# Optimization experiments

Hardware: AMD Instinct MI355X
Metric: run time of the kernel (lower is better)

## Reference

```python
import jax, jax.numpy as jnp
import numpy as np

N = 100000
E = 1600000
NEG_SLOPE = 0.2


def _gat_layer(x, src, dst, W, a_src, a_dst, b, heads, out_ch):
    n = x.shape[0]
    h = (x @ W).reshape(n, heads, out_ch)                      # [N,H,C]
    alpha_src = (h * a_src).sum(-1)                            # [N,H]
    alpha_dst = (h * a_dst).sum(-1)                            # [N,H]
    e = jax.nn.leaky_relu(alpha_src[src] + alpha_dst[dst], NEG_SLOPE)  # [E,H]
    # segment softmax over incoming edges of each destination node
    m = jax.ops.segment_max(e, dst, num_segments=n)            # [N,H]
    ex = jnp.exp(e - m[dst])
    denom = jax.ops.segment_sum(ex, dst, num_segments=n)       # [N,H]
    alpha = ex / (denom[dst] + 1e-16)                          # [E,H]
    msg = h[src] * alpha[:, :, None]                           # [E,H,C]
    out = jax.ops.segment_sum(msg, dst, num_segments=n)        # [N,H,C]
    return out.reshape(n, heads * out_ch) + b


def setup_inputs() -> dict:
    key = jax.random.key(0)
    ks = jax.random.split(key, 10)
    glorot = lambda k, shape: jax.random.normal(k, shape, jnp.float32) * np.sqrt(2.0 / (shape[0] + shape[-1]))
    x = jax.random.normal(ks[0], (N, 5), jnp.float32)
    edge_index = jax.random.randint(ks[1], (2, E), 0, N, jnp.int64)
    return {
        "x": x,
        "edge_index": edge_index,
        "W1": glorot(ks[2], (5, 64)),
        "a_src1": glorot(ks[3], (8, 8)),
        "a_dst1": glorot(ks[4], (8, 8)),
        "b1": jnp.zeros((64,), jnp.float32),
        "W2": glorot(ks[5], (64, 2)),
        "a_src2": glorot(ks[6], (1, 2)),
        "a_dst2": glorot(ks[7], (1, 2)),
        "b2": jnp.zeros((2,), jnp.float32),
    }


def reference(x, edge_index, W1, a_src1, a_dst1, b1, W2, a_src2, a_dst2, b2):
    n = x.shape[0]
    loop = jnp.arange(n, dtype=edge_index.dtype)
    src = jnp.concatenate([edge_index[0], loop])   # PyG GATConv adds self-loops
    dst = jnp.concatenate([edge_index[1], loop])
    # dropout layers are no-ops in eval mode
    h = jax.nn.elu(_gat_layer(x, src, dst, W1, a_src1, a_dst1, b1, heads=8, out_ch=8))
    out = _gat_layer(h, src, dst, W2, a_src2, a_dst2, b2, heads=1, out_ch=2)
    return jax.nn.log_softmax(out, axis=1)
```

## Files before the change

### kernel.cpp

```cpp
#include <hip/hip_runtime.h>
#include <hip/hip_fp16.h>
#include <math.h>
#include <stdint.h>

#define N_NODES 100000
#define N_EDGES 1600000
#define NEG_SLOPE 0.2f
#define LOG2E 1.44269504088896340736f

#define CB     128
#define CBBITS 7
#define NCB    ((N_NODES + CB - 1) / CB)
#define TP     2048
#define NPB    ((N_EDGES + TP - 1) / TP)
#define WINB   2560
#define NB_NODE1 ((N_NODES * 8 + 511) / 512)
#define N8     ((size_t)N_NODES * 8)
#define NTT    25

typedef int nt_int4 __attribute__((ext_vector_type(4)));

__global__ void __launch_bounds__(512) k_np(
        const int* __restrict__ src, const int* __restrict__ dst,
        int* __restrict__ ofs, unsigned* __restrict__ pairs,
        const float* __restrict__ x, const float* __restrict__ W1,
        const float* __restrict__ a_src1, const float* __restrict__ a_dst1,
        __half* __restrict__ nd, float* __restrict__ ad1) {
    __shared__ int lcnt[1024];
    __shared__ unsigned stage[TP];
    __shared__ int wred[8];
    int t = threadIdx.x;

    if (blockIdx.x >= NPB) {
        int gid  = (blockIdx.x - NPB) * 512 + t;
        int n    = gid >> 3;
        int head = gid & 7;
        if (n >= N_NODES) return;

        float xv[5];
#pragma unroll
        for (int k = 0; k < 5; ++k) xv[k] = x[n * 5 + k];

        float as = 0.f, ad = 0.f;
#pragma unroll
        for (int j = 0; j < 8; ++j) {
            int c = head * 8 + j;
            float acc = 0.f;
#pragma unroll
            for (int k = 0; k < 5; ++k) acc += xv[k] * W1[k * 64 + c];
            as += acc * a_src1[c];
            ad += acc * a_dst1[c];
        }
        nd[(size_t)n * 16 + head] = __float2half(as * LOG2E);
        ad1[n * 8 + head] = ad * LOG2E;

        if (head == 0) {
            __half2 p0 = __halves2half2(__float2half(xv[0]), __float2half(xv[1]));
            __half2 p1 = __halves2half2(__float2half(xv[2]), __float2half(xv[3]));
            __half2 p2 = __halves2half2(__float2half(xv[4]), __float2half(0.f));
            __half2 p3 = __halves2half2(__float2half(0.f), __float2half(0.f));
            __half2* xp = (__half2*)&nd[(size_t)n * 16 + 8];
            xp[0] = p0; xp[1] = p1; xp[2] = p2; xp[3] = p3;
        }
        return;
    }

    int blk = blockIdx.x;
    int base = blk * TP + t * 4;
    bool act = base < N_EDGES;
    int nE = min(TP, N_EDGES - blk * TP);

    lcnt[t] = 0; lcnt[t + 512] = 0;
    __syncthreads();

    nt_int4 s4, d4;
    int myidx[4];
    if (act) {
        s4 = __builtin_nontemporal_load((const nt_int4*)(src + base));
        d4 = __builtin_nontemporal_load((const nt_int4*)(dst + base));
#pragma unroll
        for (int j = 0; j < 4; ++j)
            myidx[j] = atomicAdd(&lcnt[d4[j] >> CBBITS], 1);
    }
    __syncthreads();

    int b0 = lcnt[t * 2], b1 = lcnt[t * 2 + 1];
    int local = b0 + b1;
    int ln = t & 63, w = t >> 6;
    int sc = local;
#pragma unroll
    for (int off = 1; off < 64; off <<= 1) {
        int u = __shfl_up(sc, off, 64);
        if (ln >= off) sc += u;
    }
    if (ln == 63) wred[w] = sc;
    __syncthreads();
    if (t < 8) {
        int v = wred[t], s = v;
#pragma unroll
        for (int off = 1; off < 8; off <<= 1) {
            int u = __shfl_up(s, off, 8);
            if ((t & 7) >= off) s += u;
        }
        wred[t] = s - v;
    }
    __syncthreads();
    int run = wred[w] + sc - local;
    lcnt[t * 2] = run; lcnt[t * 2 + 1] = run + b0;
    int* orow = ofs + (size_t)blk * (NCB + 1);
    if (t * 2     <= NCB) orow[t * 2]     = run;
    if (t * 2 + 1 <= NCB) orow[t * 2 + 1] = run + b0;
    __syncthreads();

    if (act) {
#pragma unroll
        for (int j = 0; j < 4; ++j) {
            int d = d4[j];
            stage[lcnt[d >> CBBITS] + myidx[j]] =
                ((unsigned)(d & (CB - 1)) << 17) | (unsigned)s4[j];
        }
    }
    __syncthreads();
    for (int i = t; i < nE; i += 512)
        pairs[(size_t)blk * TP + i] = stage[i];
}

__global__ void __launch_bounds__(256) k_tr(
        const int* __restrict__ ofs, int* __restrict__ ofsT) {
    __shared__ int tile[32][33];
    int bx = blockIdx.x % NTT;
    int by = blockIdx.x / NTT;
    int tx = threadIdx.x & 31, ty = threadIdx.x >> 5;
#pragma unroll
    for (int i = 0; i < 4; ++i) {
        int r = by * 32 + ty + 8 * i;
        int c = bx * 32 + tx;
        tile[ty + 8 * i][tx] = (r < NPB && c <= NCB)
                             ? ofs[(size_t)r * (NCB + 1) + c] : 0;
    }
    __syncthreads();
#pragma unroll
    for (int i = 0; i < 4; ++i) {
        int c = bx * 32 + ty + 8 * i;
        int r = by * 32 + tx;
        if (c <= NCB && r < NPB)
            ofsT[(size_t)c * NPB + r] = tile[tx][ty + 8 * i];
    }
}

__global__ void __launch_bounds__(512) k_csr(
        const int* __restrict__ ofsT, const unsigned* __restrict__ pairs,
        int* __restrict__ rbeg, int* __restrict__ rend, int* __restrict__ ssrc) {
    __shared__ unsigned stIn[WINB];
    __shared__ int stOut[WINB];
    __shared__ unsigned short sliceId[WINB];
    __shared__ int o0s[NPB];
    __shared__ int cns[1026];
    __shared__ int lcnt[CB], lofs[CB], lcur[CB];
    __shared__ int wsum[2];
    __shared__ int wred[8];
    int B = blockIdx.x, t = threadIdx.x;
    int nvalid = min(CB, N_NODES - B * CB);
    int obase = B * WINB;

    for (int s = t; s < NPB; s += 512) {
        int o0 = ofsT[(size_t)B       * NPB + s];
        int o1 = ofsT[(size_t)(B + 1) * NPB + s];
        o0s[s] = o0;
        cns[s] = o1 - o0;
    }
    for (int s = NPB + t; s < 1024; s += 512) cns[s] = 0;
    if (t < CB) {
        lcnt[t] = (t < nvalid) ? 1 : 0;
        lcur[t] = 1;
    }
    __syncthreads();

    int a0 = cns[t * 2], a1 = cns[t * 2 + 1];
    int local = a0 + a1;
    int ln = t & 63, w = t >> 6;
    int sc2 = local;
#pragma unroll
    for (int off = 1; off < 64; off <<= 1) {
        int u = __shfl_up(sc2, off, 64);
        if (ln >= off) sc2 += u;
    }
    if (ln == 63) wred[w] = sc2;
    __syncthreads();
    if (t < 8) {
        int v = wred[t], s = v;
#pragma unroll
        for (int off = 1; off < 8; off <<= 1) {
            int u = __shfl_up(s, off, 8);
            if ((t & 7) >= off) s += u;
        }
        wred[t] = s - v;
    }
    __syncthreads();
    int run = wred[w] + sc2 - local;
    cns[t * 2] = run; cns[t * 2 + 1] = run + a0;
    __syncthreads();
    int m = cns[NPB];

    for (int s = t; s < NPB; s += 512) {
        int j0 = cns[s], j1 = cns[s + 1];
        for (int j = j0; j < j1; ++j) sliceId[j] = (unsigned short)s;
    }
    __syncthreads();

    for (int i = t; i < m; i += 512) {
        int s = sliceId[i];
        unsigned r = pairs[(size_t)s * TP + o0s[s] + (i - cns[s])];
        stIn[i] = r;
        atomicAdd(&lcnt[r >> 17], 1);
    }
    __syncthreads();

    int v = (t < CB) ? lcnt[t] : 0;
    int wv = t >> 6;
    int sc = v;
#pragma unroll
    for (int off = 1; off < 64; off <<= 1) {
        int u = __shfl_up(sc, off, 64);
        if (ln >= off) sc += u;
    }
    if (ln == 63 && wv < 2) wsum[wv] = sc;
    __syncthreads();
    int wbase = (wv == 1) ? wsum[0] : 0;
    int ex = wbase + sc - v;
    if (t < CB) {
        lofs[t] = ex;
        int gi = B * CB + t;
        if (gi < N_NODES) {
            rbeg[gi] = obase + ex;
            rend[gi] = obase + ex + v;
            stOut[ex] = gi;
        }
    }
    __syncthreads();

    for (int k = t; k < m; k += 512) {
        unsigned p = stIn[k];
        int dl = p >> 17;
        int idx = atomicAdd(&lcur[dl], 1);
        stOut[lofs[dl] + idx] = (int)(p & 0x1FFFF);
    }
    __syncthreads();

    int tot = m + nvalid;
    for (int i = t; i < tot; i += 512) ssrc[obase + i] = stOut[i];
}

__global__ void __launch_bounds__(256) k_gather1(
        const int* __restrict__ rbeg, const int* __restrict__ rend,
        const int* __restrict__ ssrc, const __half* __restrict__ nd,
        const float* __restrict__ ad1, float* __restrict__ xsbuf) {
    int gtid = blockIdx.x * blockDim.x + threadIdx.x;
    int d      = gtid >> 4;
    int lane16 = threadIdx.x & 15;
    if (d >= N_NODES) return;
    int e = lane16 >> 3;
    int h = lane16 & 7;

    int beg = rbeg[d], end = rend[d];
    float adv = ad1[d * 8 + h];
    float c0 = 0.f, c1 = 0.f, c2 = 0.f, c3 = 0.f, c4 = 0.f, den = 0.f;

    for (int k = beg; k < end; k += 4) {
        int kA = k + e, kB = k + 2 + e;
        bool vA = kA < end, vB = kB < end;
        int sA = ssrc[vA ? kA : beg];
        int sB = ssrc[vB ? kB : beg];
        float eA = __half2float(nd[(size_t)sA * 16 + h]);
        float eB = __half2float(nd[(size_t)sB * 16 + h]);
        float4 xA = *(const float4*)(nd + (size_t)sA * 16 + 8);
        float4 xB = *(const float4*)(nd + (size_t)sB * 16 + 8);
        float tA = eA + adv; tA = fmaxf(tA, NEG_SLOPE * tA);
        float tB = eB + adv; tB = fmaxf(tB, NEG_SLOPE * tB);
        float wA = vA ? __builtin_amdgcn_exp2f(tA) : 0.f;
        float wB = vB ? __builtin_amdgcn_exp2f(tB) : 0.f;
        float2 A01 = __half22float2(*(__half2*)&xA.x);
        float2 A23 = __half22float2(*(__half2*)&xA.y);
        float2 A4_ = __half22float2(*(__half2*)&xA.z);
        float2 B01 = __half22float2(*(__half2*)&xB.x);
        float2 B23 = __half22float2(*(__half2*)&xB.y);
        float2 B4_ = __half22float2(*(__half2*)&xB.z);
        c0 += wA * A01.x + wB * B01.x;
        c1 += wA * A01.y + wB * B01.y;
        c2 += wA * A23.x + wB * B23.x;
        c3 += wA * A23.y + wB * B23.y;
        c4 += wA * A4_.x + wB * B4_.x;
        den += wA + wB;
    }

#define REDH(x) x += __shfl_xor(x, 8, 64);
    REDH(c0) REDH(c1) REDH(c2) REDH(c3) REDH(c4) REDH(den)
#undef REDH

    if (e == 0) {
        float inv = 1.f / den;
        size_t idx = (size_t)d * 8 + h;
        xsbuf[idx]          = c0 * inv;
        xsbuf[N8 + idx]     = c1 * inv;
        xsbuf[2 * N8 + idx] = c2 * inv;
        xsbuf[3 * N8 + idx] = c3 * inv;
        xsbuf[4 * N8 + idx] = c4 * inv;
    }
}

__global__ void __launch_bounds__(256) k_rec(
        const float* __restrict__ xsbuf, const float* __restrict__ b1,
        const float* __restrict__ W1, const float* __restrict__ W2,
        const float* __restrict__ a_src2, const float* __restrict__ a_dst2,
        float4* __restrict__ rec) {
    int gtid = blockIdx.x * blockDim.x + threadIdx.x;
    int d = gtid >> 3;
    int h = gtid & 7;
    if (d >= N_NODES) return;

    size_t idx = (size_t)d * 8 + h;
    float xs[5] = { xsbuf[idx], xsbuf[N8 + idx], xsbuf[2 * N8 + idx],
                    xsbuf[3 * N8 + idx], xsbuf[4 * N8 + idx] };

    float4 hA = ((const float4*)b1)[2 * h];
    float4 hB = ((const float4*)b1)[2 * h + 1];
#pragma unroll
    for (int c = 0; c < 5; ++c) {
        float xc = xs[c];
        float4 wA = *(const float4*)(W1 + c * 64 + 8 * h);
        float4 wB = *(const float4*)(W1 + c * 64 + 8 * h + 4);
        hA.x += xc * wA.x; hA.y += xc * wA.y; hA.z += xc * wA.z; hA.w += xc * wA.w;
        hB.x += xc * wB.x; hB.y += xc * wB.y; hB.z += xc * wB.z; hB.w += xc * wB.w;
    }
    float v0 = hA.x, v1 = hA.y, v2 = hA.z, v3 = hA.w;
    float v4 = hB.x, v5 = hB.y, v6 = hB.z, v7 = hB.w;
    v0 = (v0 > 0.f) ? v0 : (__expf(v0) - 1.f);
    v1 = (v1 > 0.f) ? v1 : (__expf(v1) - 1.f);
    v2 = (v2 > 0.f) ? v2 : (__expf(v2) - 1.f);
    v3 = (v3 > 0.f) ? v3 : (__expf(v3) - 1.f);
    v4 = (v4 > 0.f) ? v4 : (__expf(v4) - 1.f);
    v5 = (v5 > 0.f) ? v5 : (__expf(v5) - 1.f);
    v6 = (v6 > 0.f) ? v6 : (__expf(v6) - 1.f);
    v7 = (v7 > 0.f) ? v7 : (__expf(v7) - 1.f);

    const float4* w4 = (const float4*)(W2 + h * 16);
    float4 wq0 = w4[0], wq1 = w4[1], wq2 = w4[2], wq3 = w4[3];
    float h20 = v0 * wq0.x + v1 * wq0.z + v2 * wq1.x + v3 * wq1.z
              + v4 * wq2.x + v5 * wq2.z + v6 * wq3.x + v7 * wq3.z;
    float h21 = v0 * wq0.y + v1 * wq0.w + v2 * wq1.y + v3 * wq1.w
              + v4 * wq2.y + v5 * wq2.w + v6 * wq3.y + v7 * wq3.w;
    h20 += __shfl_xor(h20, 1, 64); h20 += __shfl_xor(h20, 2, 64); h20 += __shfl_xor(h20, 4, 64);
    h21 += __shfl_xor(h21, 1, 64); h21 += __shfl_xor(h21, 2, 64); h21 += __shfl_xor(h21, 4, 64);

    if (h == 0) {
        float as2v = (h20 * a_src2[0] + h21 * a_src2[1]) * LOG2E;
        float ad2v = (h20 * a_dst2[0] + h21 * a_dst2[1]) * LOG2E;
        rec[d] = make_float4(h20, h21, as2v, ad2v);
    }
}

__global__ void __launch_bounds__(256) k_gather2(
        const int* __restrict__ rbeg, const int* __restrict__ rend,
        const int* __restrict__ ssrc, const float4* __restrict__ rec,
        const float* __restrict__ b2, float* __restrict__ out) {
    int gtid = blockIdx.x * blockDim.x + threadIdx.x;
    int d    = gtid >> 3;
    int lane = threadIdx.x & 7;
    if (d >= N_NODES) return;

    int beg = rbeg[d], end = rend[d];
    float adv = rec[d].w;
    float n0 = 0.f, n1 = 0.f, den = 0.f;
    for (int k = beg; k < end; k += 8) {
        int ki = k + lane;
        bool v = ki < end;
        int s = ssrc[v ? ki : beg];
        float4 r = rec[s];
        float t = r.z + adv; t = fmaxf(t, NEG_SLOPE * t);
        float w = v ? __builtin_amdgcn_exp2f(t) : 0.f;
        n0 += w * r.x; n1 += w * r.y; den += w;
    }
#pragma unroll
    for (int off = 1; off < 8; off <<= 1) {
        n0  += __shfl_xor(n0,  off, 8);
        n1  += __shfl_xor(n1,  off, 8);
        den += __shfl_xor(den, off, 8);
    }
    if (lane == 0) {
        float o0 = n0 / den + b2[0];
        float o1 = n1 / den + b2[1];
        float m  = fmaxf(o0, o1);
        float lse = m + __logf(__expf(o0 - m) + __expf(o1 - m));
        *(float2*)(out + (size_t)d * 2) = make_float2(o0 - lse, o1 - lse);
    }
}

extern "C" void kernel_launch(void* const* d_in, const int* in_sizes, int n_in,
                              void* d_out, int out_size, void* d_ws, size_t ws_size,
                              hipStream_t stream) {
    const float* x      = (const float*)d_in[0];
    const int*   ei     = (const int*)d_in[1];
    const float* W1     = (const float*)d_in[2];
    const float* a_src1 = (const float*)d_in[3];
    const float* a_dst1 = (const float*)d_in[4];
    const float* b1     = (const float*)d_in[5];
    const float* W2     = (const float*)d_in[6];
    const float* a_src2 = (const float*)d_in[7];
    const float* a_dst2 = (const float*)d_in[8];
    const float* b2     = (const float*)d_in[9];
    float* out = (float*)d_out;

    const int* src = ei;
    const int* dst = ei + N_EDGES;

    int* rbeg   = (int*)d_ws;
    int* rend   = rbeg + N_NODES;
    int* ssrc   = rend + N_NODES;
    uintptr_t pp = ((uintptr_t)(ssrc + (size_t)NCB * WINB) + 255) & ~(uintptr_t)255;
    float4*   rec  = (float4*)pp;
    float*    ad1  = (float*)(rec + N_NODES);
    __half*   nd   = (__half*)(ad1 + (size_t)N_NODES * 8);
    uintptr_t rg = ((uintptr_t)(nd + (size_t)N_NODES * 16) + 255) & ~(uintptr_t)255;
    int*      ofs   = (int*)rg;
    int*      ofsT  = ofs + (size_t)NPB * (NCB + 1);
    unsigned* pairs = (unsigned*)(ofsT + (size_t)(NCB + 1) * NPB);
    float*    xsbuf = (float*)rg;

    k_np<<<NPB + NB_NODE1, 512, 0, stream>>>(src, dst, ofs, pairs,
                                             x, W1, a_src1, a_dst1,
                                             nd, ad1);
    k_tr<<<NTT * NTT, 256, 0, stream>>>(ofs, ofsT);
    k_csr<<<NCB, 512, 0, stream>>>(ofsT, pairs, rbeg, rend, ssrc);
    k_gather1<<<(N_NODES * 16 + 255) / 256, 256, 0, stream>>>(rbeg, rend, ssrc,
                                                              nd, ad1, xsbuf);
    k_rec<<<(N_NODES * 8 + 255) / 256, 256, 0, stream>>>(xsbuf, b1, W1, W2,
                                                         a_src2, a_dst2, rec);
    k_gather2<<<(N_NODES * 8 + 255) / 256, 256, 0, stream>>>(rbeg, rend, ssrc,
                                                             rec, b2, out);
}
```

Before: 153.9 us.

## Drop offset transpose kernel and fuse layer-2 projection into gather1

Removes the transpose kernel, so k_csr reads the per-block offset table with strided accesses instead of the transposed copy. Fuses the k_rec computation (bias, ELU, W2 projection, attention scores) into the end of k_gather1. This drops the 5-plane xsbuf intermediate and two launches. The costs are uncoalesced strided offset reads in k_csr, and every gather1 lane pair now repeats the epilogue, which raises register pressure.

```diff
diff --git a/kernel.cpp b/kernel.cpp
--- a/kernel.cpp
+++ b/kernel.cpp
@@ -15,8 +15,6 @@
 #define NPB    ((N_EDGES + TP - 1) / TP)
 #define WINB   2560
 #define NB_NODE1 ((N_NODES * 8 + 511) / 512)
-#define N8     ((size_t)N_NODES * 8)
-#define NTT    25
 
 typedef int nt_int4 __attribute__((ext_vector_type(4)));
 
@@ -125,31 +123,8 @@
         pairs[(size_t)blk * TP + i] = stage[i];
 }
 
-__global__ void __launch_bounds__(256) k_tr(
-        const int* __restrict__ ofs, int* __restrict__ ofsT) {
-    __shared__ int tile[32][33];
-    int bx = blockIdx.x % NTT;
-    int by = blockIdx.x / NTT;
-    int tx = threadIdx.x & 31, ty = threadIdx.x >> 5;
-#pragma unroll
-    for (int i = 0; i < 4; ++i) {
-        int r = by * 32 + ty + 8 * i;
-        int c = bx * 32 + tx;
-        tile[ty + 8 * i][tx] = (r < NPB && c <= NCB)
-                             ? ofs[(size_t)r * (NCB + 1) + c] : 0;
-    }
-    __syncthreads();
-#pragma unroll
-    for (int i = 0; i < 4; ++i) {
-        int c = bx * 32 + ty + 8 * i;
-        int r = by * 32 + tx;
-        if (c <= NCB && r < NPB)
-            ofsT[(size_t)c * NPB + r] = tile[tx][ty + 8 * i];
-    }
-}
-
 __global__ void __launch_bounds__(512) k_csr(
-        const int* __restrict__ ofsT, const unsigned* __restrict__ pairs,
+        const int* __restrict__ ofs, const unsigned* __restrict__ pairs,
         int* __restrict__ rbeg, int* __restrict__ rend, int* __restrict__ ssrc) {
     __shared__ unsigned stIn[WINB];
     __shared__ int stOut[WINB];
@@ -164,8 +139,9 @@
     int obase = B * WINB;
 
     for (int s = t; s < NPB; s += 512) {
-        int o0 = ofsT[(size_t)B       * NPB + s];
-        int o1 = ofsT[(size_t)(B + 1) * NPB + s];
+        const int* orow = ofs + (size_t)s * (NCB + 1) + B;
+        int o0 = orow[0];
+        int o1 = orow[1];
         o0s[s] = o0;
         cns[s] = o1 - o0;
     }
@@ -254,7 +230,10 @@
 __global__ void __launch_bounds__(256) k_gather1(
         const int* __restrict__ rbeg, const int* __restrict__ rend,
         const int* __restrict__ ssrc, const __half* __restrict__ nd,
-        const float* __restrict__ ad1, float* __restrict__ xsbuf) {
+        const float* __restrict__ ad1, const float* __restrict__ b1,
+        const float* __restrict__ W1, const float* __restrict__ W2,
+        const float* __restrict__ a_src2, const float* __restrict__ a_dst2,
+        float4* __restrict__ rec) {
     int gtid = blockIdx.x * blockDim.x + threadIdx.x;
     int d      = gtid >> 4;
     int lane16 = threadIdx.x & 15;
@@ -297,30 +276,8 @@
     REDH(c0) REDH(c1) REDH(c2) REDH(c3) REDH(c4) REDH(den)
 #undef REDH
 
-    if (e == 0) {
-        float inv = 1.f / den;
-        size_t idx = (size_t)d * 8 + h;
-        xsbuf[idx]          = c0 * inv;
-        xsbuf[N8 + idx]     = c1 * inv;
-        xsbuf[2 * N8 + idx] = c2 * inv;
-        xsbuf[3 * N8 + idx] = c3 * inv;
-        xsbuf[4 * N8 + idx] = c4 * inv;
-    }
-}
-
-__global__ void __launch_bounds__(256) k_rec(
-        const float* __restrict__ xsbuf, const float* __restrict__ b1,
-        const float* __restrict__ W1, const float* __restrict__ W2,
-        const float* __restrict__ a_src2, const float* __restrict__ a_dst2,
-        float4* __restrict__ rec) {
-    int gtid = blockIdx.x * blockDim.x + threadIdx.x;
-    int d = gtid >> 3;
-    int h = gtid & 7;
-    if (d >= N_NODES) return;
-
-    size_t idx = (size_t)d * 8 + h;
-    float xs[5] = { xsbuf[idx], xsbuf[N8 + idx], xsbuf[2 * N8 + idx],
-                    xsbuf[3 * N8 + idx], xsbuf[4 * N8 + idx] };
+    float inv = 1.f / den;
+    float xs[5] = { c0 * inv, c1 * inv, c2 * inv, c3 * inv, c4 * inv };
 
     float4 hA = ((const float4*)b1)[2 * h];
     float4 hB = ((const float4*)b1)[2 * h + 1];
@@ -352,7 +309,7 @@
     h20 += __shfl_xor(h20, 1, 64); h20 += __shfl_xor(h20, 2, 64); h20 += __shfl_xor(h20, 4, 64);
     h21 += __shfl_xor(h21, 1, 64); h21 += __shfl_xor(h21, 2, 64); h21 += __shfl_xor(h21, 4, 64);
 
-    if (h == 0) {
+    if (lane16 == 0) {
         float as2v = (h20 * a_src2[0] + h21 * a_src2[1]) * LOG2E;
         float ad2v = (h20 * a_dst2[0] + h21 * a_dst2[1]) * LOG2E;
         rec[d] = make_float4(h20, h21, as2v, ad2v);
@@ -422,19 +379,15 @@
     __half*   nd   = (__half*)(ad1 + (size_t)N_NODES * 8);
     uintptr_t rg = ((uintptr_t)(nd + (size_t)N_NODES * 16) + 255) & ~(uintptr_t)255;
     int*      ofs   = (int*)rg;
-    int*      ofsT  = ofs + (size_t)NPB * (NCB + 1);
-    unsigned* pairs = (unsigned*)(ofsT + (size_t)(NCB + 1) * NPB);
-    float*    xsbuf = (float*)rg;
+    unsigned* pairs = (unsigned*)(ofs + (size_t)NPB * (NCB + 1));
 
     k_np<<<NPB + NB_NODE1, 512, 0, stream>>>(src, dst, ofs, pairs,
                                              x, W1, a_src1, a_dst1,
                                              nd, ad1);
-    k_tr<<<NTT * NTT, 256, 0, stream>>>(ofs, ofsT);
-    k_csr<<<NCB, 512, 0, stream>>>(ofsT, pairs, rbeg, rend, ssrc);
+    k_csr<<<NCB, 512, 0, stream>>>(ofs, pairs, rbeg, rend, ssrc);
     k_gather1<<<(N_NODES * 16 + 255) / 256, 256, 0, stream>>>(rbeg, rend, ssrc,
-                                                              nd, ad1, xsbuf);
-    k_rec<<<(N_NODES * 8 + 255) / 256, 256, 0, stream>>>(xsbuf, b1, W1, W2,
-                                                         a_src2, a_dst2, rec);
+                                                              nd, ad1, b1, W1, W2,
+                                                              a_src2, a_dst2, rec);
     k_gather2<<<(N_NODES * 8 + 255) / 256, 256, 0, stream>>>(rbeg, rend, ssrc,
                                                              rec, b2, out);
 }
```

New measurement: 152.6 us. About the same (-0.8%).
